# Optimization experiments

Hardware: AMD Instinct MI355X
Metric: run time of the kernel (lower is better)

The kernel has to match this reference:

```python
import jax, jax.numpy as jnp
import numpy as np

T, H, I, E, K = 1024, 1024, 512, 32, 4   # tokens, hidden, moe_inter, n_experts, top_k
G, TG, NS = 8, 4, 2                      # n_group, topk_group, n_shared_experts
C = 2 * T * K // E                       # expert capacity (no-drop headroom)
SCALE = 2.5                              # routed_scaling_factor


def setup_inputs() -> dict:
    key = jax.random.key(0)
    ks = jax.random.split(key, 7)
    s = 0.02
    return dict(
        hidden_states=jax.random.normal(ks[0], (T, H), jnp.float32),
        gate_w=jax.random.normal(ks[1], (E, H), jnp.float32) * s,
        e_bias=jax.random.normal(ks[2], (E,), jnp.float32) * 0.1,
        w_gate_up=jax.random.normal(ks[3], (E, 2 * I, H), jnp.float32) * s,
        w_down=jax.random.normal(ks[4], (E, H, I), jnp.float32) * s,
        w_gate_up_shared=jax.random.normal(ks[5], (2 * I * NS, H), jnp.float32) * s,
        w_down_shared=jax.random.normal(ks[6], (H, I * NS), jnp.float32) * s,
    )


def reference(hidden_states, gate_w, e_bias, w_gate_up, w_down, w_gate_up_shared, w_down_shared):
    x = hidden_states                                   # (T, H)
    # --- gate + sigmoid scoring (noaux_tc) ---
    logits = x @ gate_w.T                               # (T, E)
    scores = jax.nn.sigmoid(logits.astype(jnp.float32))
    sfc = scores + e_bias                               # scores_for_choice
    # --- group-limited top-k: top-2 sum per group, keep topk_group groups ---
    group_scores = jax.lax.top_k(sfc.reshape(T, G, E // G), 2)[0].sum(-1)  # (T, G)
    grp_idx = jax.lax.top_k(group_scores, TG)[1]        # (T, TG)
    gmask = jnp.zeros((T, G), jnp.float32).at[jnp.arange(T)[:, None], grp_idx].set(1.0)
    smask = jnp.repeat(gmask, E // G, axis=1)           # (T, E)
    sfc_m = jnp.where(smask > 0, sfc, 0.0)
    topk_idx = jax.lax.top_k(sfc_m, K)[1]               # (T, K)
    tw = jnp.take_along_axis(scores, topk_idx, axis=1)  # weights from raw scores
    tw = tw / (tw.sum(-1, keepdims=True) + 1e-20)       # norm_topk_prob
    tw = tw * SCALE
    # --- capacity-based dispatch (position within expert via cumsum of one-hot) ---
    e_flat = topk_idx.reshape(-1)                       # (T*K,)
    oh = jax.nn.one_hot(e_flat, E, dtype=jnp.float32)   # (T*K, E)
    pos = jnp.sum((jnp.cumsum(oh, axis=0) - 1.0) * oh, axis=-1).astype(jnp.int32)
    keep = (pos < C).astype(jnp.float32)                # capacity sized to never drop
    pos_c = jnp.clip(pos, 0, C - 1)
    t_flat = jnp.repeat(jnp.arange(T), K)
    combine = jnp.zeros((T, E, C), jnp.float32).at[t_flat, e_flat, pos_c].add(tw.reshape(-1) * keep)
    dispatch = jnp.zeros((T, E, C), jnp.float32).at[t_flat, e_flat, pos_c].add(keep)
    # --- grouped expert MLP (gate_up -> SiluAndMul -> down) ---
    xe = jnp.einsum('tec,th->ech', dispatch, x)         # (E, C, H)
    gu = jnp.einsum('ech,eoh->eco', xe, w_gate_up)      # (E, C, 2I)
    act = jax.nn.silu(gu[..., :I]) * gu[..., I:]
    ye = jnp.einsum('eci,ehi->ech', act, w_down)        # (E, C, H)
    routed = jnp.einsum('tec,ech->th', combine, ye)     # (T, H)
    # --- shared experts MLP on residual ---
    IS = I * NS
    gus = x @ w_gate_up_shared.T                        # (T, 2*IS)
    acts = jax.nn.silu(gus[:, :IS]) * gus[:, IS:]
    shared = acts @ w_down_shared.T                     # (T, H)
    return routed + shared
```

## Files before the change

### kernel.cpp

```cpp
#include <hip/hip_runtime.h>
#include <hip/hip_bf16.h>
#include <math.h>

#define T_TOK 1024
#define H_DIM 1024
#define I_DIM 512
#define E_NUM 32
#define K_TOP 4
#define G_NUM 8
#define TG_NUM 4
#define CAP 256
#define IS_DIM 1024
#define RSCALE 2.5f

#define MAXTILES 160

#define WS_CNT_OFF    0
#define WS_NT_OFF     128
#define WS_TILE_OFF   256
#define WS_EIDX_OFF   4096
#define WS_WN_OFF     20480
#define WS_STOK_OFF   36864
#define WS_SW_OFF     69632
#define WS_ACT_OFF    102400
#define WS_ACTS_OFF   (102400 + (size_t)E_NUM*CAP*I_DIM*2)

typedef __attribute__((ext_vector_type(8))) short short8v;
typedef __attribute__((ext_vector_type(4))) float f32x4;
typedef __attribute__((ext_vector_type(4))) unsigned uint4v;

__device__ __forceinline__ short f2bf(float f) {
    unsigned u = __float_as_uint(f);
    u += 0x7FFFu + ((u >> 16) & 1u);
    return (short)(u >> 16);
}
__device__ __forceinline__ unsigned pk2bf(float a, float b) {
    unsigned ua = __float_as_uint(a) + 0x8000u;
    unsigned ub = __float_as_uint(b) + 0x8000u;
    return __builtin_amdgcn_perm(ub, ua, 0x07060302);
}
__device__ __forceinline__ uint4v pk8bf(float4 lo, float4 hi) {
    uint4v r; r.x = pk2bf(lo.x, lo.y); r.y = pk2bf(lo.z, lo.w);
    r.z = pk2bf(hi.x, hi.y); r.w = pk2bf(hi.z, hi.w); return r;
}
__device__ __forceinline__ float silu_(float g) { return g / (1.f + expf(-g)); }

#define LDSTRIDE 40

__global__ __launch_bounds__(256) void gate_kernel(
    const float* __restrict__ x, const float* __restrict__ gate_w,
    const float* __restrict__ e_bias,
    int* __restrict__ eidx, float* __restrict__ wnorm)
{
    __shared__ float xs[H_DIM];
    __shared__ float logits[E_NUM];
    const int t = blockIdx.x;
    const int tid = threadIdx.x;
    ((float4*)xs)[tid] = ((const float4*)(x + (size_t)t * H_DIM))[tid];
    __syncthreads();

    const int e = tid >> 3, sub = tid & 7;
    const float4* gw4 = (const float4*)(gate_w + (size_t)e * H_DIM + sub * 128);
    const float4* xr4 = (const float4*)(xs + sub * 128);
    float p = 0.f;
    #pragma unroll
    for (int h = 0; h < 32; ++h) {
        float4 a = xr4[h], b = gw4[h];
        p += a.x * b.x + a.y * b.y + a.z * b.z + a.w * b.w;
    }
    for (int off = 4; off; off >>= 1) p += __shfl_down(p, off, 8);
    if (sub == 0) logits[e] = p;
    __syncthreads();
    if (tid != 0) return;

    float sc[E_NUM], sfc[E_NUM];
    for (int i = 0; i < E_NUM; ++i) {
        sc[i] = 1.f / (1.f + expf(-logits[i]));
        sfc[i] = sc[i] + e_bias[i];
    }
    float gs[G_NUM];
    for (int g = 0; g < G_NUM; ++g) {
        float m1 = -1e30f, m2 = -1e30f;
        for (int j = 0; j < E_NUM / G_NUM; ++j) {
            float v = sfc[g * (E_NUM / G_NUM) + j];
            if (v > m1) { m2 = m1; m1 = v; } else if (v > m2) m2 = v;
        }
        gs[g] = m1 + m2;
    }
    bool gm[G_NUM];
    for (int g = 0; g < G_NUM; ++g) gm[g] = false;
    for (int it = 0; it < TG_NUM; ++it) {
        int best = -1; float bv = -1e30f;
        for (int g = 0; g < G_NUM; ++g) if (!gm[g] && gs[g] > bv) { bv = gs[g]; best = g; }
        gm[best] = true;
    }
    float sm[E_NUM];
    for (int i = 0; i < E_NUM; ++i) sm[i] = gm[i / (E_NUM / G_NUM)] ? sfc[i] : 0.0f;
    int idx[K_TOP]; float w[K_TOP]; float tsum = 0.f;
    for (int it = 0; it < K_TOP; ++it) {
        int best = 0; float bv = -1e30f;
        for (int i = 0; i < E_NUM; ++i) if (sm[i] > bv) { bv = sm[i]; best = i; }
        sm[best] = -1e30f;
        idx[it] = best; w[it] = sc[best]; tsum += w[it];
    }
    float inv = RSCALE / (tsum + 1e-20f);
    const int base = t * K_TOP;
    for (int it = 0; it < K_TOP; ++it) {
        eidx[base + it] = idx[it];
        wnorm[base + it] = w[it] * inv;
    }
}

__global__ __launch_bounds__(256) void assign_kernel(
    const int* __restrict__ eidx, const float* __restrict__ wnorm,
    int* __restrict__ cnt, int* __restrict__ slot_token, float* __restrict__ slot_w,
    int* __restrict__ ntiles, int* __restrict__ tiles)
{
    __shared__ int   se[T_TOK * K_TOP];
    __shared__ float swt[T_TOK * K_TOP];
    __shared__ int   scnt[E_NUM];
    const int tid = threadIdx.x;
    for (int i = tid; i < T_TOK * K_TOP; i += 256) { se[i] = eidx[i]; swt[i] = wnorm[i]; }
    __syncthreads();

    const int e = tid >> 3;
    const int seg = tid & 7;
    const int base = seg * 512;
    int c = 0;
    for (int i = 0; i < 512; ++i) c += (se[base + i] == e);
    int excl = 0, total = 0;
    for (int s = 0; s < 8; ++s) {
        int cs = __shfl(c, s, 8);
        total += cs;
        if (s < seg) excl += cs;
    }
    if (seg == 0) { cnt[e] = total; scnt[e] = total; }
    int pos = excl;
    for (int i = 0; i < 512; ++i) {
        if (se[base + i] == e) {
            if (pos < CAP) {
                slot_token[e * CAP + pos] = (base + i) >> 2;
                slot_w[e * CAP + pos] = swt[base + i];
            }
            ++pos;
        }
    }
    __syncthreads();
    if (tid == 0) {
        int nt = 0;
        for (int t0 = 0; t0 < T_TOK; t0 += 64) {
            tiles[nt * 4] = -1; tiles[nt * 4 + 1] = t0; tiles[nt * 4 + 2] = 64; ++nt;
        }
        for (int ee = 0; ee < E_NUM; ++ee) {
            int n = min(scnt[ee], CAP);
            for (int r = 0; r < n; r += 64) {
                tiles[nt * 4] = ee; tiles[nt * 4 + 1] = r; tiles[nt * 4 + 2] = n; ++nt;
            }
        }
        *ntiles = nt;
    }
}

#define WAVE_SETUP() \
    const int tid = threadIdx.x; const int lane = tid & 63; const int wid = tid >> 6; \
    const int wm = wid & 1, wn = wid >> 1; \
    const int lr16 = lane & 15, kc = lane >> 4; \
    const int sc_ = tid & 3, srow = tid >> 2;

#define DECL_ACC() f32x4 acc[2][4]; \
    _Pragma("unroll") for (int i_ = 0; i_ < 2; ++i_) \
    _Pragma("unroll") for (int j_ = 0; j_ < 4; ++j_) acc[i_][j_] = 0.f;

#define COMPUTE_2x4(Asb, Bsb) do { \
    short8v a_[2], b_[4]; \
    _Pragma("unroll") for (int mt = 0; mt < 2; ++mt) \
        a_[mt] = *(const short8v*)&(Asb)[(wm*32 + mt*16 + lr16)*LDSTRIDE + kc*8]; \
    _Pragma("unroll") for (int nt = 0; nt < 4; ++nt) \
        b_[nt] = *(const short8v*)&(Bsb)[(wn*64 + nt*16 + lr16)*LDSTRIDE + kc*8]; \
    _Pragma("unroll") for (int mt = 0; mt < 2; ++mt) \
    _Pragma("unroll") for (int nt = 0; nt < 4; ++nt) \
        acc[mt][nt] = __builtin_amdgcn_mfma_f32_16x16x32_bf16(a_[mt], b_[nt], acc[mt][nt], 0, 0, 0); \
} while (0)

__global__ __launch_bounds__(256, 4) void gu_all_kernel(
    const float* __restrict__ x, const float* __restrict__ w_gate_up,
    const float* __restrict__ w_gus,
    const int* __restrict__ ntiles, const int* __restrict__ tiles,
    const int* __restrict__ slot_token, const float* __restrict__ slot_w,
    short* __restrict__ act, short* __restrict__ acts)
{
    if ((int)blockIdx.y >= *ntiles) return;
    const int e  = tiles[blockIdx.y * 4];
    const int r0 = tiles[blockIdx.y * 4 + 1];
    const int ne = tiles[blockIdx.y * 4 + 2];
    const bool sh = (e < 0);
    if (!sh && blockIdx.x >= I_DIM / 64) return;
    const int col0 = blockIdx.x * 64;

    __shared__ __align__(16) short As[2][64 * LDSTRIDE];
    __shared__ __align__(16) short Bs[2][128 * LDSTRIDE];
    __shared__ int   toks[64];
    __shared__ float sws[64];

    WAVE_SETUP();
    if (tid < 64) {
        if (sh) { toks[tid] = r0 + tid; sws[tid] = 1.f; }
        else {
            int p = r0 + tid; bool v = p < ne;
            toks[tid] = v ? slot_token[e * CAP + p] : 0;
            sws[tid]  = v ? slot_w[e * CAP + p] : 0.f;
        }
    }
    __syncthreads();

    const int IDim = sh ? IS_DIM : I_DIM;
    const float* wbase = sh ? w_gus : (w_gate_up + (size_t)e * (2 * I_DIM) * H_DIM);
    const int c1 = srow + 64;
    const int wr0 = ((srow >> 4) & 1) * IDim + col0 + ((srow >> 5) << 4) + (srow & 15);
    const int wr1 = ((c1 >> 4) & 1) * IDim + col0 + ((c1 >> 5) << 4) + (c1 & 15);
    const float* aptr  = x + (size_t)toks[srow] * H_DIM + sc_ * 8;
    const float* bptr0 = wbase + (size_t)wr0 * H_DIM + sc_ * 8;
    const float* bptr1 = wbase + (size_t)wr1 * H_DIM + sc_ * 8;
    const int aoff  = srow * LDSTRIDE + sc_ * 8;
    const int boff1 = c1 * LDSTRIDE + sc_ * 8;

    DECL_ACC();
    float4 cA0 = *(const float4*)(aptr),  cA1 = *(const float4*)(aptr + 4);
    float4 cB0a = *(const float4*)(bptr0), cB0b = *(const float4*)(bptr0 + 4);
    float4 cB1a = *(const float4*)(bptr1), cB1b = *(const float4*)(bptr1 + 4);

    int buf = 0;
    for (int k0 = 0; k0 < H_DIM; k0 += 32) {
        float4 nA0, nA1, nB0a, nB0b, nB1a, nB1b;
        const int k1 = k0 + 32;
        if (k1 < H_DIM) {
            nA0 = *(const float4*)(aptr + k1);   nA1 = *(const float4*)(aptr + k1 + 4);
            nB0a = *(const float4*)(bptr0 + k1); nB0b = *(const float4*)(bptr0 + k1 + 4);
            nB1a = *(const float4*)(bptr1 + k1); nB1b = *(const float4*)(bptr1 + k1 + 4);
        }
        *(uint4v*)&As[buf][aoff]  = pk8bf(cA0, cA1);
        *(uint4v*)&Bs[buf][aoff]  = pk8bf(cB0a, cB0b);
        *(uint4v*)&Bs[buf][boff1] = pk8bf(cB1a, cB1b);
        __syncthreads();
        COMPUTE_2x4(As[buf], Bs[buf]);
        buf ^= 1;
        cA0 = nA0; cA1 = nA1; cB0a = nB0a; cB0b = nB0b; cB1a = nB1a; cB1b = nB1b;
    }

    short* rowbase = sh ? (acts + (size_t)r0 * IS_DIM)
                        : (act + ((size_t)e * CAP + r0) * I_DIM);
    #pragma unroll
    for (int mt = 0; mt < 2; ++mt) {
        #pragma unroll
        for (int q = 0; q < 2; ++q) {
            f32x4 g = acc[mt][2 * q], u = acc[mt][2 * q + 1];
            int colI = col0 + wn * 32 + q * 16 + lr16;
            #pragma unroll
            for (int i = 0; i < 4; ++i) {
                int rl = wm * 32 + mt * 16 + kc * 4 + i;
                if (rl < ne - r0 || sh) {
                    float s = sws[rl];
                    rowbase[(size_t)rl * IDim + colI] = f2bf(s * silu_(g[i]) * u[i]);
                }
            }
        }
    }
}

__global__ __launch_bounds__(256, 4) void down_all_kernel(
    const short* __restrict__ act, const short* __restrict__ acts,
    const float* __restrict__ w_down, const float* __restrict__ w_ds,
    const int* __restrict__ ntiles, const int* __restrict__ tiles,
    const int* __restrict__ slot_token, float* __restrict__ out)
{
    if ((int)blockIdx.y >= *ntiles) return;
    const int e  = tiles[blockIdx.y * 4];
    const int r0 = tiles[blockIdx.y * 4 + 1];
    const int ne = tiles[blockIdx.y * 4 + 2];
    const bool sh = (e < 0);
    const int h0 = blockIdx.x * 128;

    __shared__ __align__(16) short As[2][64 * LDSTRIDE];
    __shared__ __align__(16) short Bs[2][128 * LDSTRIDE];
    __shared__ int toks[64];

    WAVE_SETUP();
    if (tid < 64) {
        if (sh) toks[tid] = r0 + tid;
        else {
            int p = r0 + tid;
            toks[tid] = (p < ne) ? slot_token[e * CAP + p] : 0;
        }
    }
    __syncthreads();

    const int Kdim = sh ? IS_DIM : I_DIM;
    const short* abase = sh ? (acts + (size_t)(r0 + srow) * IS_DIM)
                            : (act + ((size_t)e * CAP + r0 + srow) * I_DIM);
    const float* wbase = sh ? w_ds : (w_down + (size_t)e * H_DIM * I_DIM);
    const float* bptr0 = wbase + (size_t)(h0 + srow) * Kdim + sc_ * 8;
    const float* bptr1 = wbase + (size_t)(h0 + srow + 64) * Kdim + sc_ * 8;
    const short* aptr  = abase + sc_ * 8;
    const int aoff  = srow * LDSTRIDE + sc_ * 8;
    const int boff1 = (srow + 64) * LDSTRIDE + sc_ * 8;

    DECL_ACC();
    short8v cA = *(const short8v*)(aptr);
    float4 cB0a = *(const float4*)(bptr0), cB0b = *(const float4*)(bptr0 + 4);
    float4 cB1a = *(const float4*)(bptr1), cB1b = *(const float4*)(bptr1 + 4);

    int buf = 0;
    for (int k0 = 0; k0 < Kdim; k0 += 32) {
        short8v nA; float4 nB0a, nB0b, nB1a, nB1b;
        const int k1 = k0 + 32;
        if (k1 < Kdim) {
            nA = *(const short8v*)(aptr + k1);
            nB0a = *(const float4*)(bptr0 + k1); nB0b = *(const float4*)(bptr0 + k1 + 4);
            nB1a = *(const float4*)(bptr1 + k1); nB1b = *(const float4*)(bptr1 + k1 + 4);
        }
        *(short8v*)&As[buf][aoff] = cA;
        *(uint4v*)&Bs[buf][aoff]  = pk8bf(cB0a, cB0b);
        *(uint4v*)&Bs[buf][boff1] = pk8bf(cB1a, cB1b);
        __syncthreads();
        COMPUTE_2x4(As[buf], Bs[buf]);
        buf ^= 1;
        cA = nA; cB0a = nB0a; cB0b = nB0b; cB1a = nB1a; cB1b = nB1b;
    }

    #pragma unroll
    for (int mt = 0; mt < 2; ++mt) {
        #pragma unroll
        for (int i = 0; i < 4; ++i) {
            int rl = wm * 32 + mt * 16 + kc * 4 + i;
            if (rl < ne - r0 || sh) {
                float* orow = out + (size_t)toks[rl] * H_DIM + h0 + wn * 64;
                #pragma unroll
                for (int nt = 0; nt < 4; ++nt)
                    atomicAdd(&orow[nt * 16 + lr16], acc[mt][nt][i]);
            }
        }
    }
}

extern "C" void kernel_launch(void* const* d_in, const int* in_sizes, int n_in,
                              void* d_out, int out_size, void* d_ws, size_t ws_size,
                              hipStream_t stream) {
    const float* x   = (const float*)d_in[0];
    const float* gw  = (const float*)d_in[1];
    const float* eb  = (const float*)d_in[2];
    const float* wgu = (const float*)d_in[3];
    const float* wd  = (const float*)d_in[4];
    const float* wgs = (const float*)d_in[5];
    const float* wds = (const float*)d_in[6];
    float* out = (float*)d_out;
    char* ws = (char*)d_ws;

    int*   cnt    = (int*)(ws + WS_CNT_OFF);
    int*   ntiles = (int*)(ws + WS_NT_OFF);
    int*   tiles  = (int*)(ws + WS_TILE_OFF);
    int*   eidx   = (int*)(ws + WS_EIDX_OFF);
    float* wnorm  = (float*)(ws + WS_WN_OFF);
    int*   stok   = (int*)(ws + WS_STOK_OFF);
    float* sw     = (float*)(ws + WS_SW_OFF);
    short* act    = (short*)(ws + WS_ACT_OFF);
    short* acts   = (short*)(ws + WS_ACTS_OFF);

    hipMemsetAsync(out, 0, (size_t)T_TOK * H_DIM * sizeof(float), stream);
    gate_kernel<<<T_TOK, 256, 0, stream>>>(x, gw, eb, eidx, wnorm);
    assign_kernel<<<1, 256, 0, stream>>>(eidx, wnorm, cnt, stok, sw, ntiles, tiles);
    gu_all_kernel<<<dim3(IS_DIM / 64, MAXTILES), 256, 0, stream>>>(
        x, wgu, wgs, ntiles, tiles, stok, sw, act, acts);
    down_all_kernel<<<dim3(H_DIM / 128, MAXTILES), 256, 0, stream>>>(
        act, acts, wd, wds, ntiles, tiles, stok, out);
}
```

Measured before the change: 425.5 us.

## Use one 256-row tile per expert and pre-convert activations to bf16

The grouped GEMMs now give each expert a single tile of up to 256 rows, handled by 512-thread blocks with 8 waves (4 along M, 2 along N). Each fp32 weight tile is then loaded and converted to bf16 once per expert rather than once per 64-row chunk, which cuts redundant weight traffic. The gate kernel also writes a bf16 copy of x, so the gate-up kernel loads bf16 activations directly instead of converting them again in every block. The cost is far fewer blocks (36 tile rows), uneven per-expert work, and idle waves when an expert has fewer than 256 tokens, which can hurt occupancy and load balance.

```diff
diff --git a/kernel.cpp b/kernel.cpp
--- a/kernel.cpp
+++ b/kernel.cpp
@@ -13,7 +13,7 @@
 #define IS_DIM 1024
 #define RSCALE 2.5f
 
-#define MAXTILES 160
+#define MAXTILES 36
 
 #define WS_CNT_OFF    0
 #define WS_NT_OFF     128
@@ -24,6 +24,7 @@
 #define WS_SW_OFF     69632
 #define WS_ACT_OFF    102400
 #define WS_ACTS_OFF   (102400 + (size_t)E_NUM*CAP*I_DIM*2)
+#define WS_XB_OFF     (WS_ACTS_OFF + (size_t)T_TOK*IS_DIM*2)
 
 typedef __attribute__((ext_vector_type(8))) short short8v;
 typedef __attribute__((ext_vector_type(4))) float f32x4;
@@ -50,13 +51,18 @@
 __global__ __launch_bounds__(256) void gate_kernel(
     const float* __restrict__ x, const float* __restrict__ gate_w,
     const float* __restrict__ e_bias,
-    int* __restrict__ eidx, float* __restrict__ wnorm)
+    int* __restrict__ eidx, float* __restrict__ wnorm, short* __restrict__ xb)
 {
     __shared__ float xs[H_DIM];
     __shared__ float logits[E_NUM];
     const int t = blockIdx.x;
     const int tid = threadIdx.x;
-    ((float4*)xs)[tid] = ((const float4*)(x + (size_t)t * H_DIM))[tid];
+    float4 v = ((const float4*)(x + (size_t)t * H_DIM))[tid];
+    ((float4*)xs)[tid] = v;
+    {
+        unsigned* xd = (unsigned*)(xb + (size_t)t * H_DIM) + tid * 2;
+        xd[0] = pk2bf(v.x, v.y); xd[1] = pk2bf(v.z, v.w);
+    }
     __syncthreads();
 
     const int e = tid >> 3, sub = tid & 7;
@@ -82,8 +88,8 @@
     for (int g = 0; g < G_NUM; ++g) {
         float m1 = -1e30f, m2 = -1e30f;
         for (int j = 0; j < E_NUM / G_NUM; ++j) {
-            float v = sfc[g * (E_NUM / G_NUM) + j];
-            if (v > m1) { m2 = m1; m1 = v; } else if (v > m2) m2 = v;
+            float v2 = sfc[g * (E_NUM / G_NUM) + j];
+            if (v2 > m1) { m2 = m1; m1 = v2; } else if (v2 > m2) m2 = v2;
         }
         gs[g] = m1 + m2;
     }
@@ -148,42 +154,20 @@
     __syncthreads();
     if (tid == 0) {
         int nt = 0;
-        for (int t0 = 0; t0 < T_TOK; t0 += 64) {
-            tiles[nt * 4] = -1; tiles[nt * 4 + 1] = t0; tiles[nt * 4 + 2] = 64; ++nt;
+        for (int t0 = 0; t0 < T_TOK; t0 += 256) {
+            tiles[nt * 4] = -1; tiles[nt * 4 + 1] = t0; tiles[nt * 4 + 2] = 256; ++nt;
         }
         for (int ee = 0; ee < E_NUM; ++ee) {
             int n = min(scnt[ee], CAP);
-            for (int r = 0; r < n; r += 64) {
-                tiles[nt * 4] = ee; tiles[nt * 4 + 1] = r; tiles[nt * 4 + 2] = n; ++nt;
-            }
+            if (n > 0) { tiles[nt * 4] = ee; tiles[nt * 4 + 1] = 0; tiles[nt * 4 + 2] = n; ++nt; }
         }
         *ntiles = nt;
     }
 }
 
-#define WAVE_SETUP() \
-    const int tid = threadIdx.x; const int lane = tid & 63; const int wid = tid >> 6; \
-    const int wm = wid & 1, wn = wid >> 1; \
-    const int lr16 = lane & 15, kc = lane >> 4; \
-    const int sc_ = tid & 3, srow = tid >> 2;
-
-#define DECL_ACC() f32x4 acc[2][4]; \
-    _Pragma("unroll") for (int i_ = 0; i_ < 2; ++i_) \
-    _Pragma("unroll") for (int j_ = 0; j_ < 4; ++j_) acc[i_][j_] = 0.f;
-
-#define COMPUTE_2x4(Asb, Bsb) do { \
-    short8v a_[2], b_[4]; \
-    _Pragma("unroll") for (int mt = 0; mt < 2; ++mt) \
-        a_[mt] = *(const short8v*)&(Asb)[(wm*32 + mt*16 + lr16)*LDSTRIDE + kc*8]; \
-    _Pragma("unroll") for (int nt = 0; nt < 4; ++nt) \
-        b_[nt] = *(const short8v*)&(Bsb)[(wn*64 + nt*16 + lr16)*LDSTRIDE + kc*8]; \
-    _Pragma("unroll") for (int mt = 0; mt < 2; ++mt) \
-    _Pragma("unroll") for (int nt = 0; nt < 4; ++nt) \
-        acc[mt][nt] = __builtin_amdgcn_mfma_f32_16x16x32_bf16(a_[mt], b_[nt], acc[mt][nt], 0, 0, 0); \
-} while (0)
-
-__global__ __launch_bounds__(256, 4) void gu_all_kernel(
-    const float* __restrict__ x, const float* __restrict__ w_gate_up,
+
+__global__ __launch_bounds__(512, 2) void gu_all_kernel(
+    const short* __restrict__ xb, const float* __restrict__ w_gate_up,
     const float* __restrict__ w_gus,
     const int* __restrict__ ntiles, const int* __restrict__ tiles,
     const int* __restrict__ slot_token, const float* __restrict__ slot_w,
@@ -196,78 +180,107 @@
     const bool sh = (e < 0);
     if (!sh && blockIdx.x >= I_DIM / 64) return;
     const int col0 = blockIdx.x * 64;
-
-    __shared__ __align__(16) short As[2][64 * LDSTRIDE];
+    const int mchunks = (ne + 63) >> 6;
+    const int rows = mchunks << 6;
+
+    __shared__ __align__(16) short As[2][256 * LDSTRIDE];
     __shared__ __align__(16) short Bs[2][128 * LDSTRIDE];
-    __shared__ int   toks[64];
-    __shared__ float sws[64];
-
-    WAVE_SETUP();
-    if (tid < 64) {
+    __shared__ int   toks[256];
+    __shared__ float sws[256];
+
+    const int tid = threadIdx.x;
+    const int lane = tid & 63, wid = tid >> 6;
+    const int wm = wid & 3, wn = wid >> 2;
+    const int lr16 = lane & 15, kc = lane >> 4;
+    const int sc_ = tid & 3, srow = tid >> 2;
+
+    if (tid < 256) {
         if (sh) { toks[tid] = r0 + tid; sws[tid] = 1.f; }
         else {
-            int p = r0 + tid; bool v = p < ne;
-            toks[tid] = v ? slot_token[e * CAP + p] : 0;
-            sws[tid]  = v ? slot_w[e * CAP + p] : 0.f;
+            bool v = tid < ne;
+            toks[tid] = v ? slot_token[e * CAP + tid] : 0;
+            sws[tid]  = v ? slot_w[e * CAP + tid] : 0.f;
         }
     }
     __syncthreads();
 
     const int IDim = sh ? IS_DIM : I_DIM;
     const float* wbase = sh ? w_gus : (w_gate_up + (size_t)e * (2 * I_DIM) * H_DIM);
-    const int c1 = srow + 64;
-    const int wr0 = ((srow >> 4) & 1) * IDim + col0 + ((srow >> 5) << 4) + (srow & 15);
-    const int wr1 = ((c1 >> 4) & 1) * IDim + col0 + ((c1 >> 5) << 4) + (c1 & 15);
-    const float* aptr  = x + (size_t)toks[srow] * H_DIM + sc_ * 8;
-    const float* bptr0 = wbase + (size_t)wr0 * H_DIM + sc_ * 8;
-    const float* bptr1 = wbase + (size_t)wr1 * H_DIM + sc_ * 8;
-    const int aoff  = srow * LDSTRIDE + sc_ * 8;
-    const int boff1 = c1 * LDSTRIDE + sc_ * 8;
-
-    DECL_ACC();
-    float4 cA0 = *(const float4*)(aptr),  cA1 = *(const float4*)(aptr + 4);
-    float4 cB0a = *(const float4*)(bptr0), cB0b = *(const float4*)(bptr0 + 4);
-    float4 cB1a = *(const float4*)(bptr1), cB1b = *(const float4*)(bptr1 + 4);
+    const int wr = ((srow >> 4) & 1) * IDim + col0 + ((srow >> 5) << 4) + (srow & 15);
+    const float* bptr = wbase + (size_t)wr * H_DIM + sc_ * 8;
+    const bool a0v = srow < rows;
+    const bool a1v = (srow + 128) < rows;
+    const short* aptr0 = xb + (size_t)toks[srow] * H_DIM + sc_ * 8;
+    const short* aptr1 = xb + (size_t)toks[srow + 128] * H_DIM + sc_ * 8;
+    const int aoff0 = srow * LDSTRIDE + sc_ * 8;
+    const int aoff1 = (srow + 128) * LDSTRIDE + sc_ * 8;
+    const int boff  = srow * LDSTRIDE + sc_ * 8;
+
+    f32x4 acc[4][4];
+    #pragma unroll
+    for (int i = 0; i < 4; ++i)
+        #pragma unroll
+        for (int j = 0; j < 4; ++j) acc[i][j] = 0.f;
+
+    short8v cA0{}, cA1{};
+    if (a0v) cA0 = *(const short8v*)(aptr0);
+    if (a1v) cA1 = *(const short8v*)(aptr1);
+    float4 cB0 = *(const float4*)(bptr), cB1 = *(const float4*)(bptr + 4);
 
     int buf = 0;
     for (int k0 = 0; k0 < H_DIM; k0 += 32) {
-        float4 nA0, nA1, nB0a, nB0b, nB1a, nB1b;
+        short8v nA0{}, nA1{};
+        float4 nB0{}, nB1{};
         const int k1 = k0 + 32;
         if (k1 < H_DIM) {
-            nA0 = *(const float4*)(aptr + k1);   nA1 = *(const float4*)(aptr + k1 + 4);
-            nB0a = *(const float4*)(bptr0 + k1); nB0b = *(const float4*)(bptr0 + k1 + 4);
-            nB1a = *(const float4*)(bptr1 + k1); nB1b = *(const float4*)(bptr1 + k1 + 4);
-        }
-        *(uint4v*)&As[buf][aoff]  = pk8bf(cA0, cA1);
-        *(uint4v*)&Bs[buf][aoff]  = pk8bf(cB0a, cB0b);
-        *(uint4v*)&Bs[buf][boff1] = pk8bf(cB1a, cB1b);
+            if (a0v) nA0 = *(const short8v*)(aptr0 + k1);
+            if (a1v) nA1 = *(const short8v*)(aptr1 + k1);
+            nB0 = *(const float4*)(bptr + k1); nB1 = *(const float4*)(bptr + k1 + 4);
+        }
+        if (a0v) *(short8v*)&As[buf][aoff0] = cA0;
+        if (a1v) *(short8v*)&As[buf][aoff1] = cA1;
+        *(uint4v*)&Bs[buf][boff] = pk8bf(cB0, cB1);
         __syncthreads();
-        COMPUTE_2x4(As[buf], Bs[buf]);
+        if (wm < mchunks) {
+            short8v a_[4], b_[4];
+            #pragma unroll
+            for (int mt = 0; mt < 4; ++mt)
+                a_[mt] = *(const short8v*)&As[buf][(wm * 64 + mt * 16 + lr16) * LDSTRIDE + kc * 8];
+            #pragma unroll
+            for (int nt = 0; nt < 4; ++nt)
+                b_[nt] = *(const short8v*)&Bs[buf][(wn * 64 + nt * 16 + lr16) * LDSTRIDE + kc * 8];
+            #pragma unroll
+            for (int mt = 0; mt < 4; ++mt)
+                #pragma unroll
+                for (int nt = 0; nt < 4; ++nt)
+                    acc[mt][nt] = __builtin_amdgcn_mfma_f32_16x16x32_bf16(a_[mt], b_[nt], acc[mt][nt], 0, 0, 0);
+        }
         buf ^= 1;
-        cA0 = nA0; cA1 = nA1; cB0a = nB0a; cB0b = nB0b; cB1a = nB1a; cB1b = nB1b;
-    }
-
-    short* rowbase = sh ? (acts + (size_t)r0 * IS_DIM)
-                        : (act + ((size_t)e * CAP + r0) * I_DIM);
+        cA0 = nA0; cA1 = nA1; cB0 = nB0; cB1 = nB1;
+    }
+
+    if (wm >= mchunks) return;
     #pragma unroll
-    for (int mt = 0; mt < 2; ++mt) {
+    for (int mt = 0; mt < 4; ++mt) {
         #pragma unroll
         for (int q = 0; q < 2; ++q) {
             f32x4 g = acc[mt][2 * q], u = acc[mt][2 * q + 1];
-            int colI = col0 + wn * 32 + q * 16 + lr16;
+            const int colI = col0 + wn * 32 + q * 16 + lr16;
             #pragma unroll
             for (int i = 0; i < 4; ++i) {
-                int rl = wm * 32 + mt * 16 + kc * 4 + i;
-                if (rl < ne - r0 || sh) {
-                    float s = sws[rl];
-                    rowbase[(size_t)rl * IDim + colI] = f2bf(s * silu_(g[i]) * u[i]);
+                int r = wm * 64 + mt * 16 + kc * 4 + i;
+                if (r < ne) {
+                    float s = sws[r];
+                    short* dst = sh ? (acts + (size_t)(r0 + r) * IS_DIM + colI)
+                                    : (act + ((size_t)e * CAP + r) * I_DIM + colI);
+                    *dst = f2bf(s * silu_(g[i]) * u[i]);
                 }
             }
         }
     }
 }
 
-__global__ __launch_bounds__(256, 4) void down_all_kernel(
+__global__ __launch_bounds__(512, 2) void down_all_kernel(
     const short* __restrict__ act, const short* __restrict__ acts,
     const float* __restrict__ w_down, const float* __restrict__ w_ds,
     const int* __restrict__ ntiles, const int* __restrict__ tiles,
@@ -279,61 +292,88 @@
     const int ne = tiles[blockIdx.y * 4 + 2];
     const bool sh = (e < 0);
     const int h0 = blockIdx.x * 128;
-
-    __shared__ __align__(16) short As[2][64 * LDSTRIDE];
+    const int mchunks = (ne + 63) >> 6;
+    const int rows = mchunks << 6;
+
+    __shared__ __align__(16) short As[2][256 * LDSTRIDE];
     __shared__ __align__(16) short Bs[2][128 * LDSTRIDE];
-    __shared__ int toks[64];
-
-    WAVE_SETUP();
-    if (tid < 64) {
+    __shared__ int toks[256];
+
+    const int tid = threadIdx.x;
+    const int lane = tid & 63, wid = tid >> 6;
+    const int wm = wid & 3, wn = wid >> 2;
+    const int lr16 = lane & 15, kc = lane >> 4;
+    const int sc_ = tid & 3, srow = tid >> 2;
+
+    if (tid < 256) {
         if (sh) toks[tid] = r0 + tid;
-        else {
-            int p = r0 + tid;
-            toks[tid] = (p < ne) ? slot_token[e * CAP + p] : 0;
-        }
+        else    toks[tid] = (tid < ne) ? slot_token[e * CAP + tid] : 0;
     }
     __syncthreads();
 
     const int Kdim = sh ? IS_DIM : I_DIM;
-    const short* abase = sh ? (acts + (size_t)(r0 + srow) * IS_DIM)
-                            : (act + ((size_t)e * CAP + r0 + srow) * I_DIM);
+    const short* abase = sh ? (acts + (size_t)r0 * IS_DIM) : (act + (size_t)e * CAP * I_DIM);
     const float* wbase = sh ? w_ds : (w_down + (size_t)e * H_DIM * I_DIM);
-    const float* bptr0 = wbase + (size_t)(h0 + srow) * Kdim + sc_ * 8;
-    const float* bptr1 = wbase + (size_t)(h0 + srow + 64) * Kdim + sc_ * 8;
-    const short* aptr  = abase + sc_ * 8;
-    const int aoff  = srow * LDSTRIDE + sc_ * 8;
-    const int boff1 = (srow + 64) * LDSTRIDE + sc_ * 8;
-
-    DECL_ACC();
-    short8v cA = *(const short8v*)(aptr);
-    float4 cB0a = *(const float4*)(bptr0), cB0b = *(const float4*)(bptr0 + 4);
-    float4 cB1a = *(const float4*)(bptr1), cB1b = *(const float4*)(bptr1 + 4);
+    const float* bptr  = wbase + (size_t)(h0 + srow) * Kdim + sc_ * 8;
+    const bool a0v = srow < rows;
+    const bool a1v = (srow + 128) < rows;
+    const short* aptr0 = abase + (size_t)srow * Kdim + sc_ * 8;
+    const short* aptr1 = abase + (size_t)(srow + 128) * Kdim + sc_ * 8;
+    const int aoff0 = srow * LDSTRIDE + sc_ * 8;
+    const int aoff1 = (srow + 128) * LDSTRIDE + sc_ * 8;
+    const int boff  = srow * LDSTRIDE + sc_ * 8;
+
+    f32x4 acc[4][4];
+    #pragma unroll
+    for (int i = 0; i < 4; ++i)
+        #pragma unroll
+        for (int j = 0; j < 4; ++j) acc[i][j] = 0.f;
+
+    short8v cA0{}, cA1{};
+    if (a0v) cA0 = *(const short8v*)(aptr0);
+    if (a1v) cA1 = *(const short8v*)(aptr1);
+    float4 cB0 = *(const float4*)(bptr), cB1 = *(const float4*)(bptr + 4);
 
     int buf = 0;
     for (int k0 = 0; k0 < Kdim; k0 += 32) {
-        short8v nA; float4 nB0a, nB0b, nB1a, nB1b;
+        short8v nA0{}, nA1{};
+        float4 nB0{}, nB1{};
         const int k1 = k0 + 32;
         if (k1 < Kdim) {
-            nA = *(const short8v*)(aptr + k1);
-            nB0a = *(const float4*)(bptr0 + k1); nB0b = *(const float4*)(bptr0 + k1 + 4);
-            nB1a = *(const float4*)(bptr1 + k1); nB1b = *(const float4*)(bptr1 + k1 + 4);
-        }
-        *(short8v*)&As[buf][aoff] = cA;
-        *(uint4v*)&Bs[buf][aoff]  = pk8bf(cB0a, cB0b);
-        *(uint4v*)&Bs[buf][boff1] = pk8bf(cB1a, cB1b);
+            if (a0v) nA0 = *(const short8v*)(aptr0 + k1);
+            if (a1v) nA1 = *(const short8v*)(aptr1 + k1);
+            nB0 = *(const float4*)(bptr + k1); nB1 = *(const float4*)(bptr + k1 + 4);
+        }
+        if (a0v) *(short8v*)&As[buf][aoff0] = cA0;
+        if (a1v) *(short8v*)&As[buf][aoff1] = cA1;
+        *(uint4v*)&Bs[buf][boff] = pk8bf(cB0, cB1);
         __syncthreads();
-        COMPUTE_2x4(As[buf], Bs[buf]);
+        if (wm < mchunks) {
+            short8v a_[4], b_[4];
+            #pragma unroll
+            for (int mt = 0; mt < 4; ++mt)
+                a_[mt] = *(const short8v*)&As[buf][(wm * 64 + mt * 16 + lr16) * LDSTRIDE + kc * 8];
+            #pragma unroll
+            for (int nt = 0; nt < 4; ++nt)
+                b_[nt] = *(const short8v*)&Bs[buf][(wn * 64 + nt * 16 + lr16) * LDSTRIDE + kc * 8];
+            #pragma unroll
+            for (int mt = 0; mt < 4; ++mt)
+                #pragma unroll
+                for (int nt = 0; nt < 4; ++nt)
+                    acc[mt][nt] = __builtin_amdgcn_mfma_f32_16x16x32_bf16(a_[mt], b_[nt], acc[mt][nt], 0, 0, 0);
+        }
         buf ^= 1;
-        cA = nA; cB0a = nB0a; cB0b = nB0b; cB1a = nB1a; cB1b = nB1b;
-    }
-
+        cA0 = nA0; cA1 = nA1; cB0 = nB0; cB1 = nB1;
+    }
+
+    if (wm >= mchunks) return;
     #pragma unroll
-    for (int mt = 0; mt < 2; ++mt) {
+    for (int mt = 0; mt < 4; ++mt) {
         #pragma unroll
         for (int i = 0; i < 4; ++i) {
-            int rl = wm * 32 + mt * 16 + kc * 4 + i;
-            if (rl < ne - r0 || sh) {
-                float* orow = out + (size_t)toks[rl] * H_DIM + h0 + wn * 64;
+            int r = wm * 64 + mt * 16 + kc * 4 + i;
+            if (r < ne) {
+                float* orow = out + (size_t)toks[r] * H_DIM + h0 + wn * 64;
                 #pragma unroll
                 for (int nt = 0; nt < 4; ++nt)
                     atomicAdd(&orow[nt * 16 + lr16], acc[mt][nt][i]);
@@ -364,12 +404,13 @@
     float* sw     = (float*)(ws + WS_SW_OFF);
     short* act    = (short*)(ws + WS_ACT_OFF);
     short* acts   = (short*)(ws + WS_ACTS_OFF);
+    short* xb     = (short*)(ws + WS_XB_OFF);
 
     hipMemsetAsync(out, 0, (size_t)T_TOK * H_DIM * sizeof(float), stream);
-    gate_kernel<<<T_TOK, 256, 0, stream>>>(x, gw, eb, eidx, wnorm);
+    gate_kernel<<<T_TOK, 256, 0, stream>>>(x, gw, eb, eidx, wnorm, xb);
     assign_kernel<<<1, 256, 0, stream>>>(eidx, wnorm, cnt, stok, sw, ntiles, tiles);
-    gu_all_kernel<<<dim3(IS_DIM / 64, MAXTILES), 256, 0, stream>>>(
-        x, wgu, wgs, ntiles, tiles, stok, sw, act, acts);
-    down_all_kernel<<<dim3(H_DIM / 128, MAXTILES), 256, 0, stream>>>(
+    gu_all_kernel<<<dim3(IS_DIM / 64, MAXTILES), 512, 0, stream>>>(
+        xb, wgu, wgs, ntiles, tiles, stok, sw, act, acts);
+    down_all_kernel<<<dim3(H_DIM / 128, MAXTILES), 512, 0, stream>>>(
         act, acts, wd, wds, ntiles, tiles, stok, out);
 }
```

Result: slower. 437.7 us (+2.9%).
